# Kernel tuning notes

Hardware: AMD Instinct MI355X
Metric: run time of the kernel (lower is better)

Reference implementation:

```python
import jax, jax.numpy as jnp
import numpy as np

D_MODEL = 1024
NUM_HEADS = 16
D_K = D_MODEL // NUM_HEADS
B, S = 4, 2048
NEG_INF = -1.0e9  # matches torch masked_fill value


def setup_inputs() -> dict:
    key = jax.random.key(0)
    ks = jax.random.split(key, 6)
    scale = 1.0 / np.sqrt(D_MODEL)
    x = jax.random.normal(ks[0], (B, S, D_MODEL), dtype=jnp.float32)
    # causal mask, broadcast over batch and heads: [1,1,S,S]
    mask = jnp.tril(jnp.ones((S, S), dtype=jnp.int32))[None, None]
    Wq = jax.random.normal(ks[1], (D_MODEL, D_MODEL), dtype=jnp.float32) * scale
    Wk = jax.random.normal(ks[2], (D_MODEL, D_MODEL), dtype=jnp.float32) * scale
    Wv = jax.random.normal(ks[3], (D_MODEL, D_MODEL), dtype=jnp.float32) * scale
    Wo = jax.random.normal(ks[4], (D_MODEL, D_MODEL), dtype=jnp.float32) * scale
    bq = jnp.zeros((D_MODEL,), jnp.float32)
    bk = jnp.zeros((D_MODEL,), jnp.float32)
    bv = jnp.zeros((D_MODEL,), jnp.float32)
    bo = jnp.zeros((D_MODEL,), jnp.float32)
    return {"x": x, "mask": mask, "Wq": Wq, "bq": bq, "Wk": Wk, "bk": bk,
            "Wv": Wv, "bv": bv, "Wo": Wo, "bo": bo}


def reference(x, mask, Wq, bq, Wk, bk, Wv, bv, Wo, bo):
    b, s, d = x.shape
    # projections (torch Linear: y = x @ W.T + b)
    q = (x @ Wq.T + bq).reshape(b, s, NUM_HEADS, D_K).transpose(0, 2, 1, 3)  # [B,H,S,Dk]
    k = (x @ Wk.T + bk).reshape(b, s, NUM_HEADS, D_K).transpose(0, 2, 1, 3)
    v = (x @ Wv.T + bv).reshape(b, s, NUM_HEADS, D_K).transpose(0, 2, 1, 3)
    scores = jnp.einsum("bhqd,bhkd->bhqk", q, k) / jnp.sqrt(jnp.float32(D_K))
    scores = jnp.where(mask == 0, NEG_INF, scores)
    attn = jax.nn.softmax(scores, axis=-1)
    out = jnp.einsum("bhqk,bhkd->bhqd", attn, v)  # [B,H,S,Dk]
    out = out.transpose(0, 2, 1, 3).reshape(b, s, d)
    return out @ Wo.T + bo
```

## Files before the change

kernel.cpp:

```cpp
#include <hip/hip_runtime.h>
#include <hip/hip_bf16.h>

#define D_MODEL 1024
#define NUM_HEADS 16
#define DK 64
#define BATCH 4
#define SEQ 2048

typedef __hip_bfloat16 bf16;
typedef __attribute__((ext_vector_type(8))) short bf16x8;
typedef __attribute__((ext_vector_type(4))) short bf16x4;
typedef __attribute__((ext_vector_type(4))) float f32x4;

typedef __attribute__((address_space(1))) const unsigned int gu32;
typedef __attribute__((address_space(3))) unsigned int lu32;

__device__ __forceinline__ void gll16(const bf16* g, bf16* l) {
    __builtin_amdgcn_global_load_lds((gu32*)g, (lu32*)l, 16, 0, 0);
}

__global__ __launch_bounds__(256)
void cvt_bf16(const float* __restrict__ x,  const float* __restrict__ Wq,
              const float* __restrict__ Wk, const float* __restrict__ Wv,
              const float* __restrict__ Wo, bf16* __restrict__ xb,
              bf16* __restrict__ Wb)
{
    size_t v = (size_t)blockIdx.x * 256 + threadIdx.x;
    size_t e = v * 4;
    const float* src; bf16* dst; size_t off;
    if (e < 8388608) { src = x; dst = xb; off = e; }
    else {
        size_t r = e - 8388608;
        int w = (int)(r >> 20);
        off = r & 1048575;
        src = (w == 0) ? Wq : (w == 1) ? Wk : (w == 2) ? Wv : Wo;
        dst = Wb + ((size_t)w << 20);
    }
    float4 f = *(const float4*)(src + off);
    bf16 o[4] = {__float2bfloat16(f.x), __float2bfloat16(f.y),
                 __float2bfloat16(f.z), __float2bfloat16(f.w)};
    *(bf16x4*)(dst + off) = *(const bf16x4*)o;
}

__device__ __forceinline__ void stage_gll(const bf16* __restrict__ src,
                                          bf16* lds, int t, int k0)
{
    #pragma unroll
    for (int p = 0; p < 4; ++p) {
        int idx = t + p * 256;
        int row = idx >> 3, cl = idx & 7;
        int cg = cl ^ (row & 7);
        gll16(src + (size_t)row * 1024 + k0 + cg * 8, lds + idx * 8);
    }
}

__device__ __forceinline__ bf16x8 frag_ld(const bf16* lds, int row, int h, int quad) {
    return *(const bf16x8*)(lds + row * 64 + (((h << 2) + quad) ^ (row & 7)) * 8);
}

__global__ __launch_bounds__(256)
void gemm_qkv(const bf16* __restrict__ xb, const bf16* __restrict__ Wb,
              const float* __restrict__ bq, const float* __restrict__ bk,
              const float* __restrict__ bv,
              bf16* __restrict__ Q, bf16* __restrict__ Kt, bf16* __restrict__ Vtr)
{
    __shared__ bf16 As[128 * 64];
    __shared__ bf16 Bs[128 * 64];
    const int t = threadIdx.x;
    const int wave = t >> 6, lane = t & 63;
    const int quad = lane >> 4, l16 = lane & 15;
    const int wr = wave >> 1, wc = wave & 1;
    const int proj = blockIdx.x >> 3;
    const int colBase = (blockIdx.x & 7) * 128;
    const int rowBase = blockIdx.y * 128;

    const bf16* Ablk = xb + (size_t)rowBase * 1024;
    const bf16* Bblk = Wb + ((size_t)proj << 20) + (size_t)colBase * 1024;
    const float* bias = proj == 0 ? bq : (proj == 1 ? bk : bv);

    f32x4 acc[4][4];
    #pragma unroll
    for (int i = 0; i < 4; ++i)
        #pragma unroll
        for (int j = 0; j < 4; ++j) acc[i][j] = (f32x4){0.f, 0.f, 0.f, 0.f};

    for (int k0 = 0; k0 < 1024; k0 += 64) {
        stage_gll(Ablk, As, t, k0);
        stage_gll(Bblk, Bs, t, k0);
        __syncthreads();
        #pragma unroll
        for (int h = 0; h < 2; ++h) {
            bf16x8 af[4], bfr[4];
            #pragma unroll
            for (int i = 0; i < 4; ++i)
                af[i] = frag_ld(As, wr * 64 + i * 16 + l16, h, quad);
            #pragma unroll
            for (int j = 0; j < 4; ++j)
                bfr[j] = frag_ld(Bs, wc * 64 + j * 16 + l16, h, quad);
            #pragma unroll
            for (int i = 0; i < 4; ++i)
                #pragma unroll
                for (int j = 0; j < 4; ++j)
                    acc[i][j] = __builtin_amdgcn_mfma_f32_16x16x32_bf16(af[i], bfr[j],
                                                                        acc[i][j], 0, 0, 0);
        }
        __syncthreads();
    }

    #pragma unroll
    for (int i = 0; i < 4; ++i)
        #pragma unroll
        for (int rr = 0; rr < 4; ++rr) {
            int r = rowBase + wr * 64 + i * 16 + quad * 4 + rr;
            int b_ = r >> 11, s_ = r & 2047;
            #pragma unroll
            for (int j = 0; j < 4; ++j) {
                int c = colBase + wc * 64 + j * 16 + l16;
                float v = acc[i][j][rr] + bias[c];
                int h_ = c >> 6, d_ = c & 63;
                size_t bh = (size_t)(b_ * NUM_HEADS + h_);
                if (proj == 2)
                    Vtr[(bh * DK + d_) * SEQ + s_] = __float2bfloat16(v);
                else {
                    bf16* dst = proj == 0 ? Q : Kt;
                    dst[(bh * SEQ + s_) * DK + d_] = __float2bfloat16(v);
                }
            }
        }
}

__global__ __launch_bounds__(256)
void gemm_out(const bf16* __restrict__ ctx, const bf16* __restrict__ Wb,
              const float* __restrict__ bo, float* __restrict__ out)
{
    __shared__ bf16 As[128 * 64];
    __shared__ bf16 Bs[128 * 64];
    const int t = threadIdx.x;
    const int wave = t >> 6, lane = t & 63;
    const int quad = lane >> 4, l16 = lane & 15;
    const int wr = wave >> 1, wc = wave & 1;
    const int colBase = blockIdx.x * 128;
    const int rowBase = blockIdx.y * 128;

    const bf16* Ablk = ctx + (size_t)rowBase * 1024;
    const bf16* Bblk = Wb + ((size_t)3 << 20) + (size_t)colBase * 1024;

    f32x4 acc[4][4];
    #pragma unroll
    for (int i = 0; i < 4; ++i)
        #pragma unroll
        for (int j = 0; j < 4; ++j) acc[i][j] = (f32x4){0.f, 0.f, 0.f, 0.f};

    for (int k0 = 0; k0 < 1024; k0 += 64) {
        stage_gll(Ablk, As, t, k0);
        stage_gll(Bblk, Bs, t, k0);
        __syncthreads();
        #pragma unroll
        for (int h = 0; h < 2; ++h) {
            bf16x8 af[4], bfr[4];
            #pragma unroll
            for (int i = 0; i < 4; ++i)
                af[i] = frag_ld(As, wr * 64 + i * 16 + l16, h, quad);
            #pragma unroll
            for (int j = 0; j < 4; ++j)
                bfr[j] = frag_ld(Bs, wc * 64 + j * 16 + l16, h, quad);
            #pragma unroll
            for (int i = 0; i < 4; ++i)
                #pragma unroll
                for (int j = 0; j < 4; ++j)
                    acc[i][j] = __builtin_amdgcn_mfma_f32_16x16x32_bf16(af[i], bfr[j],
                                                                        acc[i][j], 0, 0, 0);
        }
        __syncthreads();
    }

    #pragma unroll
    for (int i = 0; i < 4; ++i)
        #pragma unroll
        for (int rr = 0; rr < 4; ++rr) {
            int r = rowBase + wr * 64 + i * 16 + quad * 4 + rr;
            #pragma unroll
            for (int j = 0; j < 4; ++j) {
                int c = colBase + wc * 64 + j * 16 + l16;
                out[(size_t)r * 1024 + c] = acc[i][j][rr] + bo[c];
            }
        }
}

#define AS 72

__global__ __launch_bounds__(256)
void attn_mfma(const bf16* __restrict__ Q, const bf16* __restrict__ K,
               const bf16* __restrict__ Vt, bf16* __restrict__ ctx)
{
    __shared__ bf16 Ks[64 * 64];
    __shared__ bf16 Vs[64 * 64];
    __shared__ bf16 Ps[4][16 * AS];

    const int t    = threadIdx.x;
    const int wave = t >> 6, lane = t & 63;
    const int quad = lane >> 4, l16 = lane & 15;
    const int pair = blockIdx.x;
    const int bh   = blockIdx.y;
    const int b_ = bh >> 4, h_ = bh & 15;

    const bf16* Qb = Q  + (size_t)bh * SEQ * DK;
    const bf16* Kb = K  + (size_t)bh * SEQ * DK;
    const bf16* Vb = Vt + (size_t)bh * DK * SEQ;

    const float sc = 0.125f * 1.44269504089f;

    for (int phase = 0; phase < 2; ++phase) {
        const int qbi = phase ? (31 - pair) : pair;
        const int qb  = qbi * 64;
        const int qrow0 = qb + wave * 16;

        const int qrow_frag = qrow0 + l16;
        bf16x8 qf0 = *(const bf16x8*)(Qb + (size_t)qrow_frag * DK + quad * 8);
        bf16x8 qf1 = *(const bf16x8*)(Qb + (size_t)qrow_frag * DK + 32 + quad * 8);

        f32x4 O[4];
        #pragma unroll
        for (int nc = 0; nc < 4; ++nc) O[nc] = (f32x4){0.f, 0.f, 0.f, 0.f};
        float lsum[4] = {0.f, 0.f, 0.f, 0.f};

        const int ntiles = qbi + 1;
        for (int kt = 0; kt < ntiles; ++kt) {
            const int k0 = kt * 64;
            #pragma unroll
            for (int p = 0; p < 2; ++p) {
                int idx = t + p * 256;
                int row = idx >> 3, cl = idx & 7;
                int cg = cl ^ (row & 7);
                gll16(Kb + (size_t)(k0 + row) * DK + cg * 8, Ks + idx * 8);
                gll16(Vb + (size_t)row * SEQ + k0 + cg * 8, Vs + idx * 8);
            }
            __syncthreads();

            const bool last = (kt == ntiles - 1);
            float lacc[4] = {lsum[0], lsum[1], lsum[2], lsum[3]};
            #pragma unroll
            for (int h = 0; h < 4; ++h) {
                bf16x8 kf0 = frag_ld(Ks, h * 16 + l16, 0, quad);
                bf16x8 kf1 = frag_ld(Ks, h * 16 + l16, 1, quad);
                f32x4 a = (f32x4){0.f, 0.f, 0.f, 0.f};
                a = __builtin_amdgcn_mfma_f32_16x16x32_bf16(qf0, kf0, a, 0, 0, 0);
                a = __builtin_amdgcn_mfma_f32_16x16x32_bf16(qf1, kf1, a, 0, 0, 0);
                #pragma unroll
                for (int r = 0; r < 4; ++r) {
                    float ss = a[r] * sc - 32.0f;
                    if (last && (k0 + h * 16 + l16 > qrow0 + quad * 4 + r)) ss = -1e30f;
                    float p = exp2f(ss);
                    lacc[r] += p;
                    Ps[wave][(quad * 4 + r) * AS + h * 16 + l16] = __float2bfloat16(p);
                }
            }
            #pragma unroll
            for (int r = 0; r < 4; ++r) lsum[r] = lacc[r];

            bf16x8 pf0 = *(const bf16x8*)(&Ps[wave][l16 * AS + quad * 8]);
            bf16x8 pf1 = *(const bf16x8*)(&Ps[wave][l16 * AS + 32 + quad * 8]);
            #pragma unroll
            for (int nc = 0; nc < 4; ++nc) {
                bf16x8 vf0 = frag_ld(Vs, nc * 16 + l16, 0, quad);
                bf16x8 vf1 = frag_ld(Vs, nc * 16 + l16, 1, quad);
                O[nc] = __builtin_amdgcn_mfma_f32_16x16x32_bf16(pf0, vf0, O[nc], 0, 0, 0);
                O[nc] = __builtin_amdgcn_mfma_f32_16x16x32_bf16(pf1, vf1, O[nc], 0, 0, 0);
            }
            __syncthreads();
        }

        #pragma unroll
        for (int r = 0; r < 4; ++r) {
            #pragma unroll
            for (int off = 1; off < 16; off <<= 1)
                lsum[r] += __shfl_xor(lsum[r], off, 64);
        }
        #pragma unroll
        for (int nc = 0; nc < 4; ++nc)
            #pragma unroll
            for (int r = 0; r < 4; ++r) {
                int row = qrow0 + quad * 4 + r;
                float v = O[nc][r] / lsum[r];
                ctx[((size_t)(b_ * SEQ + row)) * D_MODEL + h_ * DK + nc * 16 + l16] =
                    __float2bfloat16(v);
            }
        __syncthreads();
    }
}

extern "C" void kernel_launch(void* const* d_in, const int* in_sizes, int n_in,
                              void* d_out, int out_size, void* d_ws, size_t ws_size,
                              hipStream_t stream) {
    const float* x  = (const float*)d_in[0];
    const float* Wq = (const float*)d_in[2];
    const float* bq = (const float*)d_in[3];
    const float* Wk = (const float*)d_in[4];
    const float* bk = (const float*)d_in[5];
    const float* Wv = (const float*)d_in[6];
    const float* bv = (const float*)d_in[7];
    const float* Wo = (const float*)d_in[8];
    const float* bo = (const float*)d_in[9];
    float* out = (float*)d_out;

    const size_t per = (size_t)BATCH * NUM_HEADS * SEQ * DK;
    bf16* Q   = (bf16*)d_ws;
    bf16* Kt  = Q  + per;
    bf16* Vtr = Kt + per;
    bf16* xb  = Vtr + per;
    bf16* ctx = xb;
    bf16* Wb  = xb + per;

    hipLaunchKernelGGL(cvt_bf16, dim3(12288), dim3(256), 0, stream,
                       x, Wq, Wk, Wv, Wo, xb, Wb);

    hipLaunchKernelGGL(gemm_qkv, dim3(24, 64), dim3(256), 0, stream,
                       xb, Wb, bq, bk, bv, Q, Kt, Vtr);

    hipLaunchKernelGGL(attn_mfma, dim3(16, BATCH * NUM_HEADS), dim3(256), 0,
                       stream, Q, Kt, Vtr, ctx);

    hipLaunchKernelGGL(gemm_out, dim3(8, 64), dim3(256), 0, stream, ctx, Wb, bo, out);
}
```

Baseline: 315.2 us.

## Keep softmax probabilities in registers and use 128-key tiles in attention

The QK^T MFMA operands are swapped so each lane holds transposed score fragments. The probabilities can then be packed directly into bf16x4 A-operands for 16x16x16 PV MFMAs, removing the per-wave LDS round trip through the Ps buffer. The key/value tile is widened from 64 to 128 keys with a new XOR swizzle on the V tile, which halves the number of tile iterations and barriers. The row-sum reduction is simplified to two cross-quad shuffles. The cost is wasted masked work on diagonal tiles when the query block index is even, plus twice the LDS footprint per block, which may lower occupancy.

```diff
diff --git a/kernel.cpp b/kernel.cpp
--- a/kernel.cpp
+++ b/kernel.cpp
@@ -187,15 +187,12 @@
         }
 }
 
-#define AS 72
-
 __global__ __launch_bounds__(256)
 void attn_mfma(const bf16* __restrict__ Q, const bf16* __restrict__ K,
                const bf16* __restrict__ Vt, bf16* __restrict__ ctx)
 {
-    __shared__ bf16 Ks[64 * 64];
-    __shared__ bf16 Vs[64 * 64];
-    __shared__ bf16 Ps[4][16 * AS];
+    __shared__ bf16 Ks[128 * 64];
+    __shared__ bf16 Vs[64 * 128];
 
     const int t    = threadIdx.x;
     const int wave = t >> 6, lane = t & 63;
@@ -214,78 +211,80 @@
         const int qbi = phase ? (31 - pair) : pair;
         const int qb  = qbi * 64;
         const int qrow0 = qb + wave * 16;
-
-        const int qrow_frag = qrow0 + l16;
-        bf16x8 qf0 = *(const bf16x8*)(Qb + (size_t)qrow_frag * DK + quad * 8);
-        bf16x8 qf1 = *(const bf16x8*)(Qb + (size_t)qrow_frag * DK + 32 + quad * 8);
+        const int qlane = qrow0 + l16;
+
+        bf16x8 qf0 = *(const bf16x8*)(Qb + (size_t)qlane * DK + quad * 8);
+        bf16x8 qf1 = *(const bf16x8*)(Qb + (size_t)qlane * DK + 32 + quad * 8);
 
         f32x4 O[4];
         #pragma unroll
         for (int nc = 0; nc < 4; ++nc) O[nc] = (f32x4){0.f, 0.f, 0.f, 0.f};
-        float lsum[4] = {0.f, 0.f, 0.f, 0.f};
-
-        const int ntiles = qbi + 1;
+        float lsum = 0.f;
+
+        const int ntiles = (qbi >> 1) + 1;
         for (int kt = 0; kt < ntiles; ++kt) {
-            const int k0 = kt * 64;
-            #pragma unroll
-            for (int p = 0; p < 2; ++p) {
+            const int k0 = kt * 128;
+            #pragma unroll
+            for (int p = 0; p < 4; ++p) {
                 int idx = t + p * 256;
                 int row = idx >> 3, cl = idx & 7;
-                int cg = cl ^ (row & 7);
-                gll16(Kb + (size_t)(k0 + row) * DK + cg * 8, Ks + idx * 8);
-                gll16(Vb + (size_t)row * SEQ + k0 + cg * 8, Vs + idx * 8);
+                gll16(Kb + (size_t)(k0 + row) * DK + (cl ^ (row & 7)) * 8,
+                      Ks + idx * 8);
+            }
+            #pragma unroll
+            for (int p = 0; p < 4; ++p) {
+                int idx = t + p * 256;
+                int d = idx >> 4, c8 = idx & 15;
+                gll16(Vb + (size_t)d * SEQ + k0 + (c8 ^ (d & 7)) * 8,
+                      Vs + idx * 8);
             }
             __syncthreads();
 
-            const bool last = (kt == ntiles - 1);
-            float lacc[4] = {lsum[0], lsum[1], lsum[2], lsum[3]};
-            #pragma unroll
-            for (int h = 0; h < 4; ++h) {
+            const bool need_mask = (kt == ntiles - 1);
+            #pragma unroll
+            for (int h = 0; h < 8; ++h) {
                 bf16x8 kf0 = frag_ld(Ks, h * 16 + l16, 0, quad);
                 bf16x8 kf1 = frag_ld(Ks, h * 16 + l16, 1, quad);
                 f32x4 a = (f32x4){0.f, 0.f, 0.f, 0.f};
-                a = __builtin_amdgcn_mfma_f32_16x16x32_bf16(qf0, kf0, a, 0, 0, 0);
-                a = __builtin_amdgcn_mfma_f32_16x16x32_bf16(qf1, kf1, a, 0, 0, 0);
+                a = __builtin_amdgcn_mfma_f32_16x16x32_bf16(kf0, qf0, a, 0, 0, 0);
+                a = __builtin_amdgcn_mfma_f32_16x16x32_bf16(kf1, qf1, a, 0, 0, 0);
+                bf16 pb[4];
                 #pragma unroll
                 for (int r = 0; r < 4; ++r) {
-                    float ss = a[r] * sc - 32.0f;
-                    if (last && (k0 + h * 16 + l16 > qrow0 + quad * 4 + r)) ss = -1e30f;
-                    float p = exp2f(ss);
-                    lacc[r] += p;
-                    Ps[wave][(quad * 4 + r) * AS + h * 16 + l16] = __float2bfloat16(p);
+                    float p = exp2f(a[r] * sc - 32.0f);
+                    int key = k0 + h * 16 + quad * 4 + r;
+                    if (need_mask && key > qlane) p = 0.f;
+                    lsum += p;
+                    pb[r] = __float2bfloat16(p);
                 }
-            }
-            #pragma unroll
-            for (int r = 0; r < 4; ++r) lsum[r] = lacc[r];
-
-            bf16x8 pf0 = *(const bf16x8*)(&Ps[wave][l16 * AS + quad * 8]);
-            bf16x8 pf1 = *(const bf16x8*)(&Ps[wave][l16 * AS + 32 + quad * 8]);
+                bf16x4 pa = *(const bf16x4*)pb;
+                int lc = h * 2 + (quad >> 1);
+                int c8 = (lc ^ (l16 & 7)) | (lc & 8);
+                #pragma unroll
+                for (int nc = 0; nc < 4; ++nc) {
+                    int d = nc * 16 + l16;
+                    bf16x4 vb = *(const bf16x4*)(Vs + d * 128 + c8 * 8 + (quad & 1) * 4);
+                    O[nc] = __builtin_amdgcn_mfma_f32_16x16x16bf16_1k(pa, vb, O[nc],
+                                                                      0, 0, 0);
+                }
+            }
+            __syncthreads();
+        }
+
+        lsum += __shfl_xor(lsum, 16, 64);
+        lsum += __shfl_xor(lsum, 32, 64);
+        #pragma unroll
+        for (int r = 0; r < 4; ++r) {
+            float l_r = __shfl(lsum, quad * 4 + r, 64);
+            float inv = 1.0f / l_r;
+            int row = qrow0 + quad * 4 + r;
             #pragma unroll
             for (int nc = 0; nc < 4; ++nc) {
-                bf16x8 vf0 = frag_ld(Vs, nc * 16 + l16, 0, quad);
-                bf16x8 vf1 = frag_ld(Vs, nc * 16 + l16, 1, quad);
-                O[nc] = __builtin_amdgcn_mfma_f32_16x16x32_bf16(pf0, vf0, O[nc], 0, 0, 0);
-                O[nc] = __builtin_amdgcn_mfma_f32_16x16x32_bf16(pf1, vf1, O[nc], 0, 0, 0);
-            }
-            __syncthreads();
-        }
-
-        #pragma unroll
-        for (int r = 0; r < 4; ++r) {
-            #pragma unroll
-            for (int off = 1; off < 16; off <<= 1)
-                lsum[r] += __shfl_xor(lsum[r], off, 64);
-        }
-        #pragma unroll
-        for (int nc = 0; nc < 4; ++nc)
-            #pragma unroll
-            for (int r = 0; r < 4; ++r) {
-                int row = qrow0 + quad * 4 + r;
-                float v = O[nc][r] / lsum[r];
+                float v = O[nc][r] * inv;
                 ctx[((size_t)(b_ * SEQ + row)) * D_MODEL + h_ * DK + nc * 16 + l16] =
                     __float2bfloat16(v);
             }
-        __syncthreads();
+        }
     }
 }
 
```

New measurement: 323.5 us. 2.6% more time.
